# Optimization experiments

Hardware: AMD Instinct MI355X
Metric: run time of the kernel (lower is better)

Reference implementation:

```python
import jax, jax.numpy as jnp
import numpy as np

S_IN = 14; KERNEL = 3; STRIDE = 1; C_IN = 32; C_OUT = 32; BATCH = 4; ROUTINGS = 3
EPS = 1e-7

def _child_parent_map(size_in, kernel, stride):
    # Same construction as BaseCaps._generate_voting_map: for each output position,
    # the flattened indices of its kernel window in the size_in x size_in grid.
    rows = []
    for row in range(0, size_in - kernel + 1, stride):
        for col in range(0, size_in - kernel + 1, stride):
            w = []
            for kr in range(kernel):
                start = (row + kr) * size_in + col
                w.extend(range(start, start + kernel))
            rows.append(w)
    return np.array(rows, dtype=np.int32)  # [size_out^2, kernel^2]

def setup_inputs() -> dict:
    key = jax.random.key(0)
    ks = jax.random.split(key, 5)
    in_act = jax.random.uniform(ks[0], (BATCH, S_IN, S_IN, C_IN, 1), jnp.float32)
    in_pose = jax.random.normal(ks[1], (BATCH, S_IN, S_IN, C_IN, 4, 4), jnp.float32)
    W = jax.random.normal(ks[2], (KERNEL * KERNEL * C_IN, C_OUT, 4, 4), jnp.float32) * 0.1
    beta_v = jax.random.normal(ks[3], (C_OUT,), jnp.float32)
    beta_a = jax.random.normal(ks[4], (C_OUT,), jnp.float32)
    cpm = jnp.asarray(_child_parent_map(S_IN, KERNEL, STRIDE))
    return {"in_act": in_act, "in_pose": in_pose, "transformation_weights": W,
            "beta_a": beta_a, "beta_v": beta_v, "child_parent_map": cpm}

def em_routing(act, votes, beta_a, beta_v, routings):
    # act: [B,P,K,1,1]  votes: [B,P,K,C,16]
    B, P, K, C, D = votes.shape
    rr = jnp.full((B, P, K, C, 1), 1.0 / C, votes.dtype)
    it_min, it_max = 1.0, max(1.0, min(float(routings), 3.0))
    out_a = out_mu = None
    for i in range(routings):
        inv_temp = it_min + (it_max - it_min) * (i / max(1.0, routings - 1.0))
        # --- M-step ---
        rp = rr * act                                        # [B,P,K,C,1]
        rs = rp.sum(axis=2, keepdims=True) + EPS             # [B,P,1,C,1]
        mu = (rp * votes).sum(axis=2, keepdims=True) / rs    # [B,P,1,C,D]
        var = (rp * (votes - mu) ** 2).sum(axis=2, keepdims=True) / rs + EPS
        cost = (beta_v[:, None] + 0.5 * jnp.log(var)) * rs   # [B,P,1,C,D]
        out_a = jax.nn.sigmoid(inv_temp * (beta_a[:, None] - cost.sum(-1, keepdims=True)))
        # --- E-step ---
        if i < routings - 1:
            log_p = -0.5 * jnp.sum(jnp.log(2.0 * jnp.pi * var) + (votes - mu) ** 2 / var,
                                   axis=-1, keepdims=True)   # [B,P,K,C,1]
            rr = jax.nn.softmax(jnp.log(out_a + EPS) + log_p, axis=3)
        out_mu = mu
    return out_a[:, :, 0, :, 0], out_mu[:, :, 0]  # [B,P,C], [B,P,C,D]

def reference(in_act, in_pose, transformation_weights, beta_a, beta_v, child_parent_map):
    B, S, _, Cin, _ = in_act.shape
    P, Kw = child_parent_map.shape           # [out_spatial^2, kernel^2]
    Sout = int(round(P ** 0.5))
    C = transformation_weights.shape[1]
    act = in_act.reshape(B, S * S, Cin)
    pose = in_pose.reshape(B, S * S, Cin, 4, 4)
    # gather kernel windows of child capsules per output position
    act_g = act[:, child_parent_map].reshape(B, P, Kw * Cin)             # [B,P,K]
    pose_g = pose[:, child_parent_map].reshape(B, P, Kw * Cin, 4, 4)     # [B,P,K,4,4]
    # votes = child_pose @ W, per (child k, parent capsule c)
    votes = jnp.einsum('bpkij,kcjl->bpkcil', pose_g, transformation_weights)
    votes = votes.reshape(B, P, Kw * Cin, C, 16)
    out_a, out_mu = em_routing(act_g[..., None, None], votes, beta_a, beta_v, ROUTINGS)
    out_act = out_a.reshape(B, Sout, Sout, C, 1)
    out_pose = out_mu.reshape(B, Sout, Sout, C, 4, 4)
    return out_act, out_pose
```

## Files before the change

kernel.cpp:

```cpp
#include <hip/hip_runtime.h>
#include <math.h>

#define NB 4
#define NP 144
#define KW 9
#define CIN 32
#define NC 32
#define NK 288
#define ND 16
#define EPSI 1e-7f
#define NT 512
#define NSL 16
#define KPT 18
#define NWAVES 8


template<int CTRL>
__device__ __forceinline__ float dppf(float x) {
    return __int_as_float(__builtin_amdgcn_update_dpp(
        0, __float_as_int(x), CTRL, 0xF, 0xF, true));
}
__device__ __forceinline__ float swz16(float x) {
    return __int_as_float(__builtin_amdgcn_ds_swizzle(__float_as_int(x), 0x401F));
}
__device__ __forceinline__ float red32_max(float x) {
    x = fmaxf(x, dppf<0xB1>(x));
    x = fmaxf(x, dppf<0x4E>(x));
    x = fmaxf(x, dppf<0x141>(x));
    x = fmaxf(x, dppf<0x140>(x));
    x = fmaxf(x, swz16(x));
    return x;
}
__device__ __forceinline__ float red32_sum(float x) {
    x += dppf<0xB1>(x);
    x += dppf<0x4E>(x);
    x += dppf<0x141>(x);
    x += dppf<0x140>(x);
    x += swz16(x);
    return x;
}
__device__ __forceinline__ float red16_sum(float x) {
    x += dppf<0xB1>(x);
    x += dppf<0x4E>(x);
    x += dppf<0x141>(x);
    x += dppf<0x140>(x);
    return x;
}

__device__ __forceinline__ void load16(const float* src, float* dst) {
    const float4* s4 = (const float4*)src;
    *(float4*)&dst[0]  = s4[0];
    *(float4*)&dst[4]  = s4[1];
    *(float4*)&dst[8]  = s4[2];
    *(float4*)&dst[12] = s4[3];
}

__device__ __forceinline__ void vote44(const float* pr, const float* wr, float* vote) {
    #pragma unroll
    for (int i = 0; i < 4; ++i) {
        #pragma unroll
        for (int l = 0; l < 4; ++l) {
            float v = pr[i*4+0] * wr[0*4+l];
            v = fmaf(pr[i*4+1], wr[1*4+l], v);
            v = fmaf(pr[i*4+2], wr[2*4+l], v);
            v = fmaf(pr[i*4+3], wr[3*4+l], v);
            vote[i*4+l] = v;
        }
    }
}

__device__ __forceinline__ void reduce_finalize(
    float r0, float m1[ND], float m2[ND],
    int t, int c, int wave, int lane, float inv_temp,
    float rbeta_a, float rbeta_v,
    float (&s_m1)[NWAVES][NC][ND], float (&s_m2)[NWAVES][NC][ND], float (&s_r0)[NWAVES][NC],
    float (&s_mu)[NC][17], float (&s_ivar)[NC][17],
    float (&s_L)[NC], float (&s_A)[NC], float (&s_outa)[NC])
{
    r0 += __shfl_xor(r0, 32);
    #pragma unroll
    for (int d = 0; d < ND; ++d) {
        m1[d] += __shfl_xor(m1[d], 32);
        m2[d] += __shfl_xor(m2[d], 32);
    }
    if (lane < 32) {
        float4* d1 = (float4*)&s_m1[wave][c][0];
        d1[0] = *(const float4*)&m1[0];
        d1[1] = *(const float4*)&m1[4];
        d1[2] = *(const float4*)&m1[8];
        d1[3] = *(const float4*)&m1[12];
        float4* d2 = (float4*)&s_m2[wave][c][0];
        d2[0] = *(const float4*)&m2[0];
        d2[1] = *(const float4*)&m2[4];
        d2[2] = *(const float4*)&m2[8];
        d2[3] = *(const float4*)&m2[12];
        s_r0[wave][c] = r0;
    }
    __syncthreads();

    {
        const int cc = t >> 4;
        const int d  = t & 15;
        float am1 = 0.0f, am2 = 0.0f, ar0 = 0.0f;
        #pragma unroll
        for (int g = 0; g < NWAVES; ++g) {
            am1 += s_m1[g][cc][d];
            am2 += s_m2[g][cc][d];
            ar0 += s_r0[g][cc];
        }
        const float rs  = ar0 + EPSI;
        const float irs = __builtin_amdgcn_rcpf(rs);
        const float mu  = am1 * irs;
        const float var = (am2 - mu * (2.0f * am1 - mu * ar0)) * irs + EPSI;
        const float lv  = __logf(var);
        s_mu[cc][d]   = mu;
        s_ivar[cc][d] = __builtin_amdgcn_rcpf(var);
        const float Ls = red16_sum(lv);
        if (d == 0) s_L[cc] = Ls;
    }
    __syncthreads();

    if (t < NC) {
        const float log2pi16 = 16.0f * 1.8378770664093453f;
        float ar0 = 0.0f;
        #pragma unroll
        for (int g = 0; g < NWAVES; ++g) ar0 += s_r0[g][t];
        const float rs = ar0 + EPSI;
        const float L  = s_L[t];
        const float costsum = rs * (16.0f * rbeta_v + 0.5f * L);
        const float x  = inv_temp * (rbeta_a - costsum);
        const float oa = 1.0f / (1.0f + __expf(-x));
        s_outa[t] = oa;
        s_A[t] = __logf(oa + EPSI) - 0.5f * (log2pi16 + L);
    }
    __syncthreads();
}

__global__ __launch_bounds__(NT, 2) void convcaps_em_kernel(
    const float* __restrict__ g_act,
    const float* __restrict__ g_pose,
    const float* __restrict__ g_W,
    const float* __restrict__ g_beta_a,
    const float* __restrict__ g_beta_v,
    const int*   __restrict__ g_cpm,
    float* __restrict__ g_out)
{
    __shared__ float s_pose[NK][ND];
    __shared__ float s_act[NK];
    __shared__ float s_m1[NWAVES][NC][ND];
    __shared__ float s_m2[NWAVES][NC][ND];
    __shared__ float s_r0[NWAVES][NC];
    __shared__ float s_mu[NC][17];
    __shared__ float s_ivar[NC][17];
    __shared__ float s_L[NC];
    __shared__ float s_A[NC];
    __shared__ float s_outa[NC];
    __shared__ int   s_win[KW];

    const int bp   = blockIdx.x;
    const int b    = bp / NP;
    const int p    = bp - b * NP;
    const int t    = threadIdx.x;
    const int c    = t & 31;
    const int s    = t >> 5;
    const int wave = t >> 6;
    const int lane = t & 63;

    float rbeta_a = 0.0f, rbeta_v = 0.0f;
    if (t < KW) s_win[t] = g_cpm[p * KW + t];
    if (t < NC) { rbeta_a = g_beta_a[t]; rbeta_v = g_beta_v[t]; }
    __syncthreads();

    {
        const float4* pb4 = (const float4*)(g_pose + (size_t)b * (196 * CIN * ND));
        float4* sp4 = (float4*)&s_pose[0][0];
        for (int i4 = t; i4 < NK * ND / 4; i4 += NT) {
            const int w   = i4 >> 7;
            const int rem = i4 & 127;
            sp4[i4] = pb4[(size_t)s_win[w] * 128 + rem];
        }
        const float* ab = g_act + (size_t)b * (196 * CIN);
        if (t < NK) s_act[t] = ab[s_win[t >> 5] * CIN + (t & 31)];
    }
    __syncthreads();

    const int    k0  = s * KPT;
    const float* wp0 = g_W + (size_t)(k0 * NC + c) * ND;

    {
        float r0 = 0.0f, m1[ND], m2[ND];
        #pragma unroll
        for (int d = 0; d < ND; ++d) { m1[d] = 0.0f; m2[d] = 0.0f; }

        const float* wp = wp0;
        for (int j = 0; j < KPT; ++j, wp += NC * ND) {
            const int k = k0 + j;
            float pr[ND], wr[ND], vote[ND];
            load16(&s_pose[k][0], pr);
            load16(wp, wr);
            vote44(pr, wr, vote);

            const float rp = s_act[k] * (1.0f / 32.0f);
            r0 += rp;
            #pragma unroll
            for (int d = 0; d < ND; ++d) {
                const float rv = rp * vote[d];
                m1[d] += rv;
                m2[d] = fmaf(rv, vote[d], m2[d]);
            }
        }
        reduce_finalize(r0, m1, m2, t, c, wave, lane, 1.0f, rbeta_a, rbeta_v,
                        s_m1, s_m2, s_r0, s_mu, s_ivar, s_L, s_A, s_outa);
    }

    for (int it = 1; it < 3; ++it) {
        float iv_r[ND], h2n_r[ND];
        float gq = 0.0f;
        #pragma unroll
        for (int d = 0; d < ND; ++d) {
            const float mu = s_mu[c][d];
            const float iv = s_ivar[c][d];
            iv_r[d] = iv;
            const float h = iv * mu;
            h2n_r[d] = -(h + h);
            gq = fmaf(h, mu, gq);
        }
        const float Abase = s_A[c] - 0.5f * gq;

        float r0 = 0.0f, m1[ND], m2[ND];
        #pragma unroll
        for (int d = 0; d < ND; ++d) { m1[d] = 0.0f; m2[d] = 0.0f; }

        const float* wp = wp0;
        for (int j = 0; j < KPT; ++j, wp += NC * ND) {
            const int k = k0 + j;
            float pr[ND], wr[ND], v[ND];
            load16(&s_pose[k][0], pr);
            load16(wp, wr);
            vote44(pr, wr, v);

            float q = 0.0f;
            #pragma unroll
            for (int d = 0; d < ND; ++d) {
                const float tq = fmaf(iv_r[d], v[d], h2n_r[d]);
                q = fmaf(tq, v[d], q);
            }
            const float logit = fmaf(-0.5f, q, Abase);

            const float mx = red32_max(logit);
            const float e  = __expf(logit - mx);
            const float se = red32_sum(e);

            const float rp = e * __builtin_amdgcn_rcpf(se) * s_act[k];
            r0 += rp;
            #pragma unroll
            for (int d = 0; d < ND; ++d) {
                const float rv = rp * v[d];
                m1[d] += rv;
                m2[d] = fmaf(rv, v[d], m2[d]);
            }
        }
        reduce_finalize(r0, m1, m2, t, c, wave, lane, 1.0f + (float)it, rbeta_a, rbeta_v,
                        s_m1, s_m2, s_r0, s_mu, s_ivar, s_L, s_A, s_outa);
    }

    const int base = (b * NP + p) * NC;
    if (t < NC) g_out[base + t] = s_outa[t];
    float* outpose = g_out + NB * NP * NC;
    {
        const int cc = t >> 4;
        const int d  = t & 15;
        outpose[(size_t)(base + cc) * ND + d] = s_mu[cc][d];
    }
}

extern "C" void kernel_launch(void* const* d_in, const int* in_sizes, int n_in,
                              void* d_out, int out_size, void* d_ws, size_t ws_size,
                              hipStream_t stream) {
    const float* in_act  = (const float*)d_in[0];
    const float* in_pose = (const float*)d_in[1];
    const float* W       = (const float*)d_in[2];
    const float* beta_a  = (const float*)d_in[3];
    const float* beta_v  = (const float*)d_in[4];
    const int*   cpm     = (const int*)d_in[5];
    float* out = (float*)d_out;

    convcaps_em_kernel<<<dim3(NB * NP), dim3(NT), 0, stream>>>(
        in_act, in_pose, W, beta_a, beta_v, cpm, out);
}
```

Baseline: 111.5 us.

## Halve shared reduction buffers via two-phase accumulate, swizzle, drop window staging

Cross-wave partial sums now go into half as many shared-memory slots: the upper four waves write first, then after a barrier the lower four waves add their partials in place. The float4 slots are XOR-swizzled by capsule index to cut LDS bank conflicts, and the reader applies the same mapping. The window-index staging array and its barrier are removed in favour of direct global reads, and the separate L and output-activation arrays are folded into s_A. The smaller shared footprint may allow more blocks per CU, at the cost of an extra barrier and a read-modify-write in every reduction.

Result: no change. 111.4 us (-0.1%).

```diff
diff --git a/kernel.cpp b/kernel.cpp
--- a/kernel.cpp
+++ b/kernel.cpp
@@ -10,9 +10,8 @@
 #define ND 16
 #define EPSI 1e-7f
 #define NT 512
-#define NSL 16
 #define KPT 18
-#define NWAVES 8
+#define NRED 4
 
 
 template<int CTRL>
@@ -47,6 +46,8 @@
     return x;
 }
 
+__device__ __forceinline__ int sw4(int c, int j) { return j ^ ((c >> 1) & 3); }
+
 __device__ __forceinline__ void load16(const float* src, float* dst) {
     const float4* s4 = (const float4*)src;
     *(float4*)&dst[0]  = s4[0];
@@ -71,11 +72,10 @@
 
 __device__ __forceinline__ void reduce_finalize(
     float r0, float m1[ND], float m2[ND],
-    int t, int c, int wave, int lane, float inv_temp,
+    int t, int c, int wave, int lane, float inv_temp, bool last,
     float rbeta_a, float rbeta_v,
-    float (&s_m1)[NWAVES][NC][ND], float (&s_m2)[NWAVES][NC][ND], float (&s_r0)[NWAVES][NC],
-    float (&s_mu)[NC][17], float (&s_ivar)[NC][17],
-    float (&s_L)[NC], float (&s_A)[NC], float (&s_outa)[NC])
+    float (&s_m1)[NRED][NC][ND], float (&s_m2)[NRED][NC][ND], float (&s_r0)[NRED][NC],
+    float (&s_mu)[NC][17], float (&s_ivar)[NC][17], float (&s_A)[NC])
 {
     r0 += __shfl_xor(r0, 32);
     #pragma unroll
@@ -83,29 +83,42 @@
         m1[d] += __shfl_xor(m1[d], 32);
         m2[d] += __shfl_xor(m2[d], 32);
     }
-    if (lane < 32) {
+    if (lane < 32 && wave >= NRED) {
+        float4* d1 = (float4*)&s_m1[wave - NRED][c][0];
+        float4* d2 = (float4*)&s_m2[wave - NRED][c][0];
+        #pragma unroll
+        for (int j = 0; j < 4; ++j) {
+            d1[sw4(c, j)] = *(const float4*)&m1[4*j];
+            d2[sw4(c, j)] = *(const float4*)&m2[4*j];
+        }
+        s_r0[wave - NRED][c] = r0;
+    }
+    __syncthreads();
+    if (lane < 32 && wave < NRED) {
         float4* d1 = (float4*)&s_m1[wave][c][0];
-        d1[0] = *(const float4*)&m1[0];
-        d1[1] = *(const float4*)&m1[4];
-        d1[2] = *(const float4*)&m1[8];
-        d1[3] = *(const float4*)&m1[12];
         float4* d2 = (float4*)&s_m2[wave][c][0];
-        d2[0] = *(const float4*)&m2[0];
-        d2[1] = *(const float4*)&m2[4];
-        d2[2] = *(const float4*)&m2[8];
-        d2[3] = *(const float4*)&m2[12];
-        s_r0[wave][c] = r0;
+        #pragma unroll
+        for (int j = 0; j < 4; ++j) {
+            float4 v1 = d1[sw4(c, j)];
+            v1.x += m1[4*j]; v1.y += m1[4*j+1]; v1.z += m1[4*j+2]; v1.w += m1[4*j+3];
+            d1[sw4(c, j)] = v1;
+            float4 v2 = d2[sw4(c, j)];
+            v2.x += m2[4*j]; v2.y += m2[4*j+1]; v2.z += m2[4*j+2]; v2.w += m2[4*j+3];
+            d2[sw4(c, j)] = v2;
+        }
+        s_r0[wave][c] += r0;
     }
     __syncthreads();
 
     {
         const int cc = t >> 4;
         const int d  = t & 15;
+        const int fi = cc * ND + sw4(cc, d >> 2) * 4 + (d & 3);
         float am1 = 0.0f, am2 = 0.0f, ar0 = 0.0f;
         #pragma unroll
-        for (int g = 0; g < NWAVES; ++g) {
-            am1 += s_m1[g][cc][d];
-            am2 += s_m2[g][cc][d];
+        for (int g = 0; g < NRED; ++g) {
+            am1 += (&s_m1[g][0][0])[fi];
+            am2 += (&s_m2[g][0][0])[fi];
             ar0 += s_r0[g][cc];
         }
         const float rs  = ar0 + EPSI;
@@ -116,22 +129,19 @@
         s_mu[cc][d]   = mu;
         s_ivar[cc][d] = __builtin_amdgcn_rcpf(var);
         const float Ls = red16_sum(lv);
-        if (d == 0) s_L[cc] = Ls;
+        if (d == 0) s_A[cc] = Ls;
     }
     __syncthreads();
 
     if (t < NC) {
         const float log2pi16 = 16.0f * 1.8378770664093453f;
-        float ar0 = 0.0f;
-        #pragma unroll
-        for (int g = 0; g < NWAVES; ++g) ar0 += s_r0[g][t];
+        float ar0 = s_r0[0][t] + s_r0[1][t] + s_r0[2][t] + s_r0[3][t];
         const float rs = ar0 + EPSI;
-        const float L  = s_L[t];
+        const float L  = s_A[t];
         const float costsum = rs * (16.0f * rbeta_v + 0.5f * L);
         const float x  = inv_temp * (rbeta_a - costsum);
         const float oa = 1.0f / (1.0f + __expf(-x));
-        s_outa[t] = oa;
-        s_A[t] = __logf(oa + EPSI) - 0.5f * (log2pi16 + L);
+        s_A[t] = last ? oa : (__logf(oa + EPSI) - 0.5f * (log2pi16 + L));
     }
     __syncthreads();
 }
@@ -147,15 +157,12 @@
 {
     __shared__ float s_pose[NK][ND];
     __shared__ float s_act[NK];
-    __shared__ float s_m1[NWAVES][NC][ND];
-    __shared__ float s_m2[NWAVES][NC][ND];
-    __shared__ float s_r0[NWAVES][NC];
+    __shared__ float s_m1[NRED][NC][ND];
+    __shared__ float s_m2[NRED][NC][ND];
+    __shared__ float s_r0[NRED][NC];
     __shared__ float s_mu[NC][17];
     __shared__ float s_ivar[NC][17];
-    __shared__ float s_L[NC];
     __shared__ float s_A[NC];
-    __shared__ float s_outa[NC];
-    __shared__ int   s_win[KW];
 
     const int bp   = blockIdx.x;
     const int b    = bp / NP;
@@ -167,20 +174,19 @@
     const int lane = t & 63;
 
     float rbeta_a = 0.0f, rbeta_v = 0.0f;
-    if (t < KW) s_win[t] = g_cpm[p * KW + t];
     if (t < NC) { rbeta_a = g_beta_a[t]; rbeta_v = g_beta_v[t]; }
-    __syncthreads();
-
-    {
+
+    {
+        const int* cpm = g_cpm + p * KW;
         const float4* pb4 = (const float4*)(g_pose + (size_t)b * (196 * CIN * ND));
         float4* sp4 = (float4*)&s_pose[0][0];
         for (int i4 = t; i4 < NK * ND / 4; i4 += NT) {
             const int w   = i4 >> 7;
             const int rem = i4 & 127;
-            sp4[i4] = pb4[(size_t)s_win[w] * 128 + rem];
+            sp4[i4] = pb4[(size_t)cpm[w] * 128 + rem];
         }
         const float* ab = g_act + (size_t)b * (196 * CIN);
-        if (t < NK) s_act[t] = ab[s_win[t >> 5] * CIN + (t & 31)];
+        if (t < NK) s_act[t] = ab[cpm[t >> 5] * CIN + (t & 31)];
     }
     __syncthreads();
 
@@ -209,8 +215,8 @@
                 m2[d] = fmaf(rv, vote[d], m2[d]);
             }
         }
-        reduce_finalize(r0, m1, m2, t, c, wave, lane, 1.0f, rbeta_a, rbeta_v,
-                        s_m1, s_m2, s_r0, s_mu, s_ivar, s_L, s_A, s_outa);
+        reduce_finalize(r0, m1, m2, t, c, wave, lane, 1.0f, false, rbeta_a, rbeta_v,
+                        s_m1, s_m2, s_r0, s_mu, s_ivar, s_A);
     }
 
     for (int it = 1; it < 3; ++it) {
@@ -260,12 +266,13 @@
                 m2[d] = fmaf(rv, v[d], m2[d]);
             }
         }
-        reduce_finalize(r0, m1, m2, t, c, wave, lane, 1.0f + (float)it, rbeta_a, rbeta_v,
-                        s_m1, s_m2, s_r0, s_mu, s_ivar, s_L, s_A, s_outa);
+        reduce_finalize(r0, m1, m2, t, c, wave, lane, 1.0f + (float)it, it == 2,
+                        rbeta_a, rbeta_v,
+                        s_m1, s_m2, s_r0, s_mu, s_ivar, s_A);
     }
 
     const int base = (b * NP + p) * NC;
-    if (t < NC) g_out[base + t] = s_outa[t];
+    if (t < NC) g_out[base + t] = s_A[t];
     float* outpose = g_out + NB * NP * NC;
     {
         const int cc = t >> 4;
```
